# Kernel optimization log

Measured on AMD Instinct MI355X. Metric: run time of the kernel, lower is better.

## Reference

```python
import jax, jax.numpy as jnp
import numpy as np

B, S, D = 4, 4096, 1024
E, K, H = 8, 2, 2048


def setup_inputs() -> dict:
    key = jax.random.key(0)
    ks = jax.random.split(key, 6)
    scale_g = 1.0 / np.sqrt(D)
    scale_1 = 1.0 / np.sqrt(D)
    scale_2 = 1.0 / np.sqrt(H)
    return {
        "x": jax.random.normal(ks[0], (B, S, D), dtype=jnp.float32),
        "Wg": jax.random.uniform(ks[1], (D, E), jnp.float32, -scale_g, scale_g),
        "W1": jax.random.uniform(ks[2], (E, D, H), jnp.float32, -scale_1, scale_1),
        "b1": jax.random.uniform(ks[3], (E, H), jnp.float32, -scale_1, scale_1),
        "W2": jax.random.uniform(ks[4], (E, H, D), jnp.float32, -scale_2, scale_2),
        "b2": jax.random.uniform(ks[5], (E, D), jnp.float32, -scale_2, scale_2),
    }


def reference(x, Wg, W1, b1, W2, b2):
    # Router: softmax gate, top-k selection, renormalized combine weights
    logits = jnp.einsum("bsd,de->bse", x, Wg)          # [B,S,E]
    probs = jax.nn.softmax(logits, axis=-1)
    topv, topi = jax.lax.top_k(probs, K)                # [B,S,K]
    cw = topv / (jnp.sum(topv, axis=-1, keepdims=True) + 1e-9)
    # Per-token weight for each expert: sum over k of one_hot(idx_k)*cw_k -> [B,S,E]
    we = jnp.sum(jax.nn.one_hot(topi, E, dtype=x.dtype) * cw[..., None], axis=-2)
    # Weighted combine of per-expert FFN outputs (loop over small fixed E)
    y = jnp.zeros_like(x)
    for e in range(E):
        h = jax.nn.relu(jnp.einsum("bsd,dh->bsh", x, W1[e]) + b1[e])
        out_e = jnp.einsum("bsh,hd->bsd", h, W2[e]) + b2[e]
        y = y + we[..., e:e + 1] * out_e
    return y
```

## Files before the change

kernel.cpp:

```cpp
#include <hip/hip_runtime.h>
#include <hip/hip_bf16.h>

#define TOK 16384
#define DIM 1024
#define HID 2048
#define NEXP 8

typedef __attribute__((ext_vector_type(4))) float f32x4;
typedef __attribute__((ext_vector_type(8))) short s16x8;

__device__ __forceinline__ unsigned short f2bf(float f) {
  union { float f; unsigned u; } v; v.f = f;
  unsigned r = v.u + 0x7fffu + ((v.u >> 16) & 1u);
  return (unsigned short)(r >> 16);
}
__device__ __forceinline__ int tile_byte(int r, int kk2) {
  return (r * 128 + kk2) ^ ((r & 7) << 4);
}
__device__ __forceinline__ void gld_lds16(const void* g, void* l) {
  __builtin_amdgcn_global_load_lds(
      (const __attribute__((address_space(1))) unsigned int*)g,
      (__attribute__((address_space(3))) unsigned int*)l, 16, 0, 0);
}
__device__ __forceinline__ int xcd_swz(int p, int nwg) {
  int q = nwg >> 3, r = nwg & 7;
  int xcd = p & 7, idx = p >> 3;
  return (xcd < r ? xcd * (q + 1) : r * (q + 1) + (xcd - r) * q) + idx;
}

__global__ void wg_tr(const float* __restrict__ Wg, float* __restrict__ WgT) {
  int i = blockIdx.x * 256 + threadIdx.x;
  int e = i >> 10, dd = i & 1023;
  WgT[i] = Wg[dd * NEXP + e];
}

__global__ void prep_tiles(const float* __restrict__ src, unsigned short* __restrict__ dst,
                           int rows, int cols) {
  int ct = blockIdx.x, kb = blockIdx.y, e = blockIdx.z;
  int nct = gridDim.x, nkb = gridDim.y;
  __shared__ __align__(16) unsigned short tile[8192];
  const float* s = src + ((size_t)e * rows + kb * 64) * cols + ct * 128;
  int tid = threadIdx.x;
  #pragma unroll
  for (int it = 0; it < 8; it++) {
    int idx = it * 256 + tid;
    int kk = idx >> 5;
    int r4 = (idx & 31) * 4;
    float4 v = *(const float4*)(s + (size_t)kk * cols + r4);
    char* tb = (char*)tile;
    *(unsigned short*)(tb + tile_byte(r4 + 0, kk * 2)) = f2bf(v.x);
    *(unsigned short*)(tb + tile_byte(r4 + 1, kk * 2)) = f2bf(v.y);
    *(unsigned short*)(tb + tile_byte(r4 + 2, kk * 2)) = f2bf(v.z);
    *(unsigned short*)(tb + tile_byte(r4 + 3, kk * 2)) = f2bf(v.w);
  }
  __syncthreads();
  unsigned short* d = dst + (((size_t)e * nct + ct) * nkb + kb) * 8192;
  #pragma unroll
  for (int it = 0; it < 4; it++) {
    int o = it * 256 + tid;
    *(s16x8*)(d + o * 8) = *(const s16x8*)((const char*)tile + o * 16);
  }
}

__global__ __launch_bounds__(256)
void router_logits_cvt(const float* __restrict__ x, const float* __restrict__ WgT,
                       unsigned short* __restrict__ xbf,
                       int* __restrict__ sel, float2* __restrict__ wp) {
  int wave = threadIdx.x >> 6, lane = threadIdx.x & 63;
  int t = blockIdx.x * 4 + wave;
  const f32x4* xr = (const f32x4*)(x + (size_t)t * DIM);
  unsigned short* xb = xbf + (size_t)t * DIM;
  float acc[NEXP];
  #pragma unroll
  for (int e = 0; e < NEXP; e++) acc[e] = 0.f;
  #pragma unroll
  for (int q = 0; q < 4; q++) {
    f32x4 xv = xr[q * 64 + lane];
    ushort4 bv;
    bv.x = f2bf(xv[0]); bv.y = f2bf(xv[1]); bv.z = f2bf(xv[2]); bv.w = f2bf(xv[3]);
    *(ushort4*)(xb + (q * 64 + lane) * 4) = bv;
    #pragma unroll
    for (int e = 0; e < NEXP; e++) {
      f32x4 wv = *(const f32x4*)(WgT + (size_t)e * DIM + (q * 64 + lane) * 4);
      acc[e] = fmaf(xv[3], wv[3], fmaf(xv[2], wv[2], fmaf(xv[1], wv[1], fmaf(xv[0], wv[0], acc[e]))));
    }
  }
  #pragma unroll
  for (int e = 0; e < NEXP; e++) {
    float v = acc[e];
    #pragma unroll
    for (int off = 32; off >= 1; off >>= 1) v += __shfl_xor(v, off);
    acc[e] = v;
  }
  if (lane == 0) {
    float m = acc[0];
    #pragma unroll
    for (int e = 1; e < NEXP; e++) m = fmaxf(m, acc[e]);
    float p[NEXP], s = 0.f;
    #pragma unroll
    for (int e = 0; e < NEXP; e++) { p[e] = expf(acc[e] - m); s += p[e]; }
    float inv = 1.f / s;
    int i0 = 0; float v0 = p[0];
    #pragma unroll
    for (int e = 1; e < NEXP; e++) if (p[e] > v0) { v0 = p[e]; i0 = e; }
    int i1 = -1; float v1 = -1.f;
    #pragma unroll
    for (int e = 0; e < NEXP; e++) if (e != i0 && p[e] > v1) { v1 = p[e]; i1 = e; }
    v0 *= inv; v1 *= inv;
    float den = v0 + v1 + 1e-9f;
    sel[t] = i0 | (i1 << 4);
    wp[t] = make_float2(v0 / den, v1 / den);
  }
}

__global__ __launch_bounds__(256)
void router_scatter(const int* __restrict__ sel, const float2* __restrict__ wp,
                    int* __restrict__ counts, int* __restrict__ tok_list,
                    float* __restrict__ w_list) {
  __shared__ int lh0[4][16], lh1[4][16];
  __shared__ int bbase[16];
  int tid = threadIdx.x, wave = tid >> 6, lane = tid & 63;
  int t = blockIdx.x * 256 + tid;
  int s = sel[t];
  int b0 = s & 15;
  int b1 = 8 + ((s >> 4) & 15);
  float2 w = wp[t];
  unsigned long long lt = (lane == 63) ? ~0ull >> 1 : (((unsigned long long)1 << lane) - 1);
  int r0 = 0, r1 = 0;
  #pragma unroll
  for (int b = 0; b < 8; b++) {
    unsigned long long m0 = __ballot(b0 == b);
    if (b0 == b) r0 = __popcll(m0 & lt);
    if (lane == 0) { lh0[wave][b] = __popcll(m0); lh1[wave][b] = 0; }
  }
  #pragma unroll
  for (int b = 8; b < 16; b++) {
    unsigned long long m1 = __ballot(b1 == b);
    if (b1 == b) r1 = __popcll(m1 & lt);
    if (lane == 0) { lh1[wave][b] = __popcll(m1); lh0[wave][b] = 0; }
  }
  __syncthreads();
  if (tid < 16) {
    int h = 0;
    #pragma unroll
    for (int v = 0; v < 4; v++) h += lh0[v][tid] + lh1[v][tid];
    bbase[tid] = atomicAdd(&counts[tid], h);
  }
  __syncthreads();
  int p0 = bbase[b0] + r0;
  int p1 = bbase[b1] + r1;
  #pragma unroll
  for (int v = 0; v < 4; v++) {
    if (v < wave) { p0 += lh0[v][b0]; p1 += lh1[v][b1]; }
  }
  int e0 = b0, e1 = b1 - 8;
  tok_list[e0 * TOK + p0] = t;
  w_list[e0 * TOK + p0] = w.x;
  int q1 = TOK - 1 - p1;
  tok_list[e1 * TOK + q1] = t;
  w_list[e1 * TOK + q1] = w.y;
}

__global__ void calc_off(const int* __restrict__ counts, int* __restrict__ off) {
  if (threadIdx.x == 0 && blockIdx.x == 0) {
    int a = 0;
    for (int e = 0; e < NEXP; e++)
      for (int s = 0; s < 2; s++) {
        off[e * 2 + s] = a;
        a += (counts[s * 8 + e] + 127) & ~127;
      }
  }
}

__global__ __launch_bounds__(256, 4)
void moe_gemm1(const unsigned short* __restrict__ xbf, const unsigned short* __restrict__ w1s,
               const float* __restrict__ b1, const int* __restrict__ counts,
               const int* __restrict__ off, const int* __restrict__ tok_list,
               unsigned short* __restrict__ h_s, int ct_off, int nkbc, int nct) {
  int logical = xcd_swz(blockIdx.x, gridDim.x);
  int ct_l = logical % nct;
  int g = logical / nct;
  int e = -1, seg = 0, rt = 0, segcnt = 0, base = 0;
  #pragma unroll
  for (int zz = 0; zz < 16; zz++) {
    int ee = zz >> 1, ss = zz & 1;
    int c = counts[ss * 8 + ee];
    int nt = (c + 127) >> 7;
    if (e < 0 && g < base + nt) { e = ee; seg = ss; rt = g - base; segcnt = c; }
    base += nt;
  }
  if (e < 0) return;

  __shared__ __align__(16) unsigned short As[8192];
  __shared__ __align__(16) unsigned short Bs[8192];
  __shared__ int tokS[128];

  int tid = threadIdx.x, wave = tid >> 6, lane = tid & 63;
  int llo = lane & 15, lhi = lane >> 4;
  int wr = wave >> 1, wc = wave & 1;
  int ct_g = ct_off + ct_l;

  if (tid < 128) {
    int q = rt * 128 + tid;
    int qq = q < segcnt ? q : segcnt - 1;
    int slot = seg ? (TOK - 1 - qq) : qq;
    tokS[tid] = tok_list[e * TOK + slot];
  }
  __syncthreads();

  const char* srcA[4];
  #pragma unroll
  for (int i = 0; i < 4; i++) {
    int r = i * 32 + (tid >> 3);
    srcA[i] = (const char*)xbf + (size_t)tokS[r] * (DIM * 2) + (((tid & 7) ^ (r & 7)) * 16);
  }
  const char* gB = (const char*)(w1s + (((size_t)e * 16 + ct_g) * 16) * 8192);

  f32x4 acc[4][4];
  #pragma unroll
  for (int i = 0; i < 4; i++)
    #pragma unroll
    for (int j = 0; j < 4; j++) acc[i][j] = (f32x4){0.f, 0.f, 0.f, 0.f};

  for (int kb = 0; kb < 16; kb++) {
    #pragma unroll
    for (int i = 0; i < 4; i++)
      gld_lds16(srcA[i] + kb * 128, (char*)As + i * 4096 + wave * 1024);
    const char* gs = gB + (size_t)kb * 16384 + wave * 1024 + lane * 16;
    #pragma unroll
    for (int i = 0; i < 4; i++)
      gld_lds16(gs + i * 4096, (char*)Bs + i * 4096 + wave * 1024);
    __syncthreads();
    #pragma unroll
    for (int ks = 0; ks < 2; ks++) {
      s16x8 a[4], b[4];
      #pragma unroll
      for (int f = 0; f < 4; f++) {
        a[f] = *(const s16x8*)((const char*)As + tile_byte(wr * 64 + f * 16 + llo, ks * 64 + lhi * 16));
        b[f] = *(const s16x8*)((const char*)Bs + tile_byte(wc * 64 + f * 16 + llo, ks * 64 + lhi * 16));
      }
      #pragma unroll
      for (int fr = 0; fr < 4; fr++)
        #pragma unroll
        for (int fc = 0; fc < 4; fc++)
          acc[fr][fc] = __builtin_amdgcn_mfma_f32_16x16x32_bf16(a[fr], b[fc], acc[fr][fc], 0, 0, 0);
    }
    __syncthreads();
  }

  size_t grt = (size_t)(off[e * 2 + seg] >> 7) + rt;
  unsigned short* hb = h_s + grt * ((size_t)nkbc * 8192);
  const float* b1e = b1 + e * HID + ct_g * 128;
  #pragma unroll
  for (int fc = 0; fc < 4; fc++) {
    int col = wc * 64 + fc * 16 + llo;
    float bv = b1e[col];
    char* tb = (char*)(hb + ((size_t)(ct_l * 2 + (col >> 6))) * 8192);
    int kk2 = (col & 63) * 2;
    #pragma unroll
    for (int fr = 0; fr < 4; fr++) {
      int r0 = wr * 64 + fr * 16 + lhi * 4;
      #pragma unroll
      for (int j = 0; j < 4; j++) {
        float v = fmaxf(acc[fr][fc][j] + bv, 0.f);
        *(unsigned short*)(tb + tile_byte(r0 + j, kk2)) = f2bf(v);
      }
    }
  }
}

template<int NKBC>
__global__ __launch_bounds__(256, 4)
void moe_gemm2(const unsigned short* __restrict__ h_s, const unsigned short* __restrict__ w2s,
               const float* __restrict__ b2, const int* __restrict__ counts,
               const int* __restrict__ off, const int* __restrict__ tok_list,
               const float* __restrict__ w_list, float* __restrict__ y,
               int seg, int kb_off, int add_b2, int accum) {
  int logical = xcd_swz(blockIdx.x, gridDim.x);
  int ct = logical & 7;
  int g = logical >> 3;
  int e = -1, rt = 0, segcnt = 0, base = 0;
  #pragma unroll
  for (int ee = 0; ee < 8; ee++) {
    int c = counts[seg * 8 + ee];
    int nt = (c + 127) >> 7;
    if (e < 0 && g < base + nt) { e = ee; rt = g - base; segcnt = c; }
    base += nt;
  }
  if (e < 0) return;

  __shared__ __align__(16) unsigned short As[8192];
  __shared__ __align__(16) unsigned short Bs[8192];

  int tid = threadIdx.x, wave = tid >> 6, lane = tid & 63;
  int llo = lane & 15, lhi = lane >> 4;
  int wr = wave >> 1, wc = wave & 1;

  size_t grt = (size_t)(off[e * 2 + seg] >> 7) + rt;
  const char* gA = (const char*)(h_s + grt * ((size_t)NKBC * 8192));
  const char* gB = (const char*)(w2s + (((size_t)e * 8 + ct) * 32 + kb_off) * 8192);

  f32x4 acc[4][4];
  #pragma unroll
  for (int i = 0; i < 4; i++)
    #pragma unroll
    for (int j = 0; j < 4; j++) acc[i][j] = (f32x4){0.f, 0.f, 0.f, 0.f};

  for (int kb = 0; kb < NKBC; kb++) {
    const char* ga = gA + (size_t)kb * 16384 + wave * 1024 + lane * 16;
    const char* gb = gB + (size_t)kb * 16384 + wave * 1024 + lane * 16;
    #pragma unroll
    for (int i = 0; i < 4; i++) {
      gld_lds16(ga + i * 4096, (char*)As + i * 4096 + wave * 1024);
      gld_lds16(gb + i * 4096, (char*)Bs + i * 4096 + wave * 1024);
    }
    __syncthreads();
    #pragma unroll
    for (int ks = 0; ks < 2; ks++) {
      s16x8 a[4], b[4];
      #pragma unroll
      for (int f = 0; f < 4; f++) {
        a[f] = *(const s16x8*)((const char*)As + tile_byte(wr * 64 + f * 16 + llo, ks * 64 + lhi * 16));
        b[f] = *(const s16x8*)((const char*)Bs + tile_byte(wc * 64 + f * 16 + llo, ks * 64 + lhi * 16));
      }
      #pragma unroll
      for (int fr = 0; fr < 4; fr++)
        #pragma unroll
        for (int fc = 0; fc < 4; fc++)
          acc[fr][fc] = __builtin_amdgcn_mfma_f32_16x16x32_bf16(a[fr], b[fc], acc[fr][fc], 0, 0, 0);
    }
    __syncthreads();
  }

  const float* b2e = b2 + e * DIM + ct * 128;
  #pragma unroll
  for (int fr = 0; fr < 4; fr++) {
    #pragma unroll
    for (int j = 0; j < 4; j++) {
      int q = rt * 128 + wr * 64 + fr * 16 + lhi * 4 + j;
      if (q < segcnt) {
        int slot = seg ? (TOK - 1 - q) : q;
        int t = tok_list[e * TOK + slot];
        float w = w_list[e * TOK + slot];
        float bs = add_b2 ? w : 0.f;
        #pragma unroll
        for (int fc = 0; fc < 4; fc++) {
          int col = wc * 64 + fc * 16 + llo;
          float val = w * acc[fr][fc][j] + bs * b2e[col];
          size_t idx = (size_t)t * DIM + ct * 128 + col;
          if (accum) y[idx] += val;
          else       y[idx] = val;
        }
      }
    }
  }
}

__global__ void transpose_cvt(const float* __restrict__ src, unsigned short* __restrict__ dst,
                              int R, int C) {
  __shared__ float tile[32][33];
  int e = blockIdx.z;
  const float* s = src + (size_t)e * R * C;
  unsigned short* d = dst + (size_t)e * R * C;
  int c0 = blockIdx.x * 32, r0 = blockIdx.y * 32;
  int tx = threadIdx.x, ty = threadIdx.y;
  #pragma unroll
  for (int i = 0; i < 32; i += 8)
    tile[ty + i][tx] = s[(size_t)(r0 + ty + i) * C + c0 + tx];
  __syncthreads();
  #pragma unroll
  for (int i = 0; i < 32; i += 8)
    d[(size_t)(c0 + ty + i) * R + r0 + tx] = f2bf(tile[tx][ty + i]);
}

__global__ void router_kernel(const float* __restrict__ x, const float* __restrict__ Wg,
                              int* __restrict__ counts, int* __restrict__ tok_list,
                              float* __restrict__ w_list) {
  int wave = threadIdx.x >> 6, lane = threadIdx.x & 63;
  int t = blockIdx.x * 4 + wave;
  const float* xr = x + (size_t)t * DIM;
  float acc[NEXP];
  #pragma unroll
  for (int e = 0; e < NEXP; e++) acc[e] = 0.f;
  for (int i = 0; i < DIM / 64; i++) {
    int dd = i * 64 + lane;
    float xv = xr[dd];
    const float* wr = Wg + (size_t)dd * NEXP;
    #pragma unroll
    for (int e = 0; e < NEXP; e++) acc[e] = fmaf(xv, wr[e], acc[e]);
  }
  #pragma unroll
  for (int e = 0; e < NEXP; e++) {
    float v = acc[e];
    #pragma unroll
    for (int off = 32; off >= 1; off >>= 1) v += __shfl_xor(v, off);
    acc[e] = v;
  }
  if (lane == 0) {
    float m = acc[0];
    #pragma unroll
    for (int e = 1; e < NEXP; e++) m = fmaxf(m, acc[e]);
    float p[NEXP], s = 0.f;
    #pragma unroll
    for (int e = 0; e < NEXP; e++) { p[e] = expf(acc[e] - m); s += p[e]; }
    float inv = 1.f / s;
    int i0 = 0; float v0 = p[0];
    #pragma unroll
    for (int e = 1; e < NEXP; e++) if (p[e] > v0) { v0 = p[e]; i0 = e; }
    int i1 = -1; float v1 = -1.f;
    #pragma unroll
    for (int e = 0; e < NEXP; e++) if (e != i0 && p[e] > v1) { v1 = p[e]; i1 = e; }
    v0 *= inv; v1 *= inv;
    float den = v0 + v1 + 1e-9f;
    float w0 = v0 / den, w1 = v1 / den;
    int q0 = atomicAdd(&counts[i0], 1);
    tok_list[i0 * TOK + q0] = t;           w_list[i0 * TOK + q0] = w0;
    int q1 = atomicAdd(&counts[8 + i1], 1);
    int p1 = TOK - 1 - q1;
    tok_list[i1 * TOK + p1] = t;           w_list[i1 * TOK + p1] = w1;
  }
}

__global__ __launch_bounds__(512, 4)
void moe_ffn_kernel(const float* __restrict__ x,
                    const unsigned short* __restrict__ w1t,
                    const unsigned short* __restrict__ w2t,
                    const float* __restrict__ b1, const float* __restrict__ b2,
                    const int* __restrict__ counts, const int* __restrict__ tok_list,
                    const float* __restrict__ w_list, float* __restrict__ y) {
  int zz = blockIdx.y, e = zz & 7, seg = zz >> 3;
  int segcnt = counts[seg * 8 + e];
  int row0 = blockIdx.x * 32;
  if (row0 >= segcnt) return;
  __shared__ unsigned short Xs[32 * DIM];
  __shared__ unsigned short hsl[32 * 64];
  __shared__ int tokS[32];
  __shared__ float wS[32];
  int tid = threadIdx.x, wave = tid >> 6, lane = tid & 63;
  if (tid < 32) {
    int q = row0 + tid;
    if (q < segcnt) {
      int slot = seg ? (TOK - 1 - q) : q;
      tokS[tid] = tok_list[e * TOK + slot]; wS[tid] = w_list[e * TOK + slot];
    } else { tokS[tid] = -1; wS[tid] = 0.f; }
  }
  __syncthreads();
  #pragma unroll
  for (int it = 0; it < 8; it++) {
    int chunk = it * 512 + tid;
    int r = chunk >> 7, c = (chunk & 127) * 8;
    int tok = tokS[r];
    float4 f0 = make_float4(0.f, 0.f, 0.f, 0.f), f1 = f0;
    if (tok >= 0) {
      const float4* xp = (const float4*)(x + (size_t)tok * DIM + c);
      f0 = xp[0]; f1 = xp[1];
    }
    s16x8 bv;
    bv[0] = (short)f2bf(f0.x); bv[1] = (short)f2bf(f0.y);
    bv[2] = (short)f2bf(f0.z); bv[3] = (short)f2bf(f0.w);
    bv[4] = (short)f2bf(f1.x); bv[5] = (short)f2bf(f1.y);
    bv[6] = (short)f2bf(f1.z); bv[7] = (short)f2bf(f1.w);
    int byte = (r * DIM + c) * 2; byte ^= (r & 7) << 4;
    *(s16x8*)((char*)Xs + byte) = bv;
  }
  __syncthreads();
  int rw = wave >> 2, cw = wave & 3;
  int lhi = lane >> 4, llo = lane & 15;
  f32x4 acc[16];
  #pragma unroll
  for (int i = 0; i < 16; i++) acc[i] = (f32x4){0.f, 0.f, 0.f, 0.f};
  int arow = rw * 16 + llo;
  int abase = arow * (DIM * 2) + lhi * 16;
  int aswz = (arow & 7) << 4;
  int h_abase = arow * (64 * 2) + lhi * 16;
  const size_t eHD = (size_t)e * HID * DIM;
  const unsigned short* w2e = w2t + (size_t)e * DIM * HID;
  for (int hc = 0; hc < HID; hc += 64) {
    f32x4 c1 = (f32x4){0.f, 0.f, 0.f, 0.f};
    const unsigned short* w1p = w1t + eHD + (size_t)(hc + cw * 16 + llo) * DIM + lhi * 8;
    #pragma unroll 4
    for (int k = 0; k < DIM; k += 32) {
      s16x8 a = *(const s16x8*)((const char*)Xs + ((abase + k * 2) ^ aswz));
      s16x8 b = *(const s16x8*)(w1p + k);
      c1 = __builtin_amdgcn_mfma_f32_16x16x32_bf16(a, b, c1, 0, 0, 0);
    }
    float b1v = b1[e * HID + hc + cw * 16 + llo];
    __syncthreads();
    #pragma unroll
    for (int j = 0; j < 4; j++) {
      int r = rw * 16 + lhi * 4 + j;
      float v = fmaxf(c1[j] + b1v, 0.f);
      int byte = (r * 64 + cw * 16 + llo) * 2; byte ^= (r & 7) << 4;
      *(unsigned short*)((char*)hsl + byte) = f2bf(v);
    }
    __syncthreads();
    s16x8 a0 = *(const s16x8*)((const char*)hsl + ((h_abase + 0)  ^ aswz));
    s16x8 a1 = *(const s16x8*)((const char*)hsl + ((h_abase + 64) ^ aswz));
    const unsigned short* w2p0 = w2e + hc + lhi * 8;
    #pragma unroll 4
    for (int ctile = 0; ctile < 16; ctile++) {
      int dcol = cw * 256 + ctile * 16 + llo;
      const unsigned short* bp = w2p0 + (size_t)dcol * HID;
      s16x8 b0 = *(const s16x8*)(bp);
      s16x8 b1f = *(const s16x8*)(bp + 32);
      acc[ctile] = __builtin_amdgcn_mfma_f32_16x16x32_bf16(a0, b0, acc[ctile], 0, 0, 0);
      acc[ctile] = __builtin_amdgcn_mfma_f32_16x16x32_bf16(a1, b1f, acc[ctile], 0, 0, 0);
    }
  }
  const float* b2e = b2 + e * DIM;
  #pragma unroll
  for (int ctile = 0; ctile < 16; ctile++) {
    int dcol = cw * 256 + ctile * 16 + llo;
    float b2v = b2e[dcol];
    #pragma unroll
    for (int j = 0; j < 4; j++) {
      int r = rw * 16 + lhi * 4 + j;
      int tok = tokS[r];
      if (tok >= 0) atomicAdd(&y[(size_t)tok * DIM + dcol], wS[r] * (acc[ctile][j] + b2v));
    }
  }
}

extern "C" void kernel_launch(void* const* d_in, const int* in_sizes, int n_in,
                              void* d_out, int out_size, void* d_ws, size_t ws_size,
                              hipStream_t stream) {
  const float* x  = (const float*)d_in[0];
  const float* Wg = (const float*)d_in[1];
  const float* W1 = (const float*)d_in[2];
  const float* b1 = (const float*)d_in[3];
  const float* W2 = (const float*)d_in[4];
  const float* b2 = (const float*)d_in[5];
  float* y = (float*)d_out;
  char* ws = (char*)d_ws;

  const size_t O_COUNTS = 0;
  const size_t O_OFF    = 1024;
  const size_t O_TOK    = 2048;
  const size_t O_W      = O_TOK + (size_t)NEXP * TOK * 4;
  const size_t O_WGT    = O_W + (size_t)NEXP * TOK * 4;
  const size_t O_SEL    = O_WGT + (size_t)NEXP * DIM * 4;
  const size_t O_WP     = O_SEL + (size_t)TOK * 4;
  const size_t O_W1S    = O_WP + (size_t)TOK * 8;
  const size_t O_W2S    = O_W1S + (size_t)NEXP * 16 * 16 * 8192 * 2;
  const size_t O_XBF    = O_W2S + (size_t)NEXP * 8 * 32 * 8192 * 2;
  const size_t O_HS     = O_XBF + (size_t)TOK * DIM * 2;

  int Hc = 0;
  if (ws_size > O_HS) {
    size_t avail = ws_size - O_HS;
    for (int hc = HID; hc >= 128; hc >>= 1)
      if ((size_t)34816 * hc * 2 <= avail) { Hc = hc; break; }
  }

  if (Hc) {
    int*   counts   = (int*)(ws + O_COUNTS);
    int*   offp     = (int*)(ws + O_OFF);
    int*   tok_list = (int*)(ws + O_TOK);
    float* w_list   = (float*)(ws + O_W);
    float* WgT      = (float*)(ws + O_WGT);
    int*   sel      = (int*)(ws + O_SEL);
    float2* wp      = (float2*)(ws + O_WP);
    unsigned short* w1s = (unsigned short*)(ws + O_W1S);
    unsigned short* w2s = (unsigned short*)(ws + O_W2S);
    unsigned short* xbf = (unsigned short*)(ws + O_XBF);
    unsigned short* hs  = (unsigned short*)(ws + O_HS);

    hipMemsetAsync(counts, 0, 2048, stream);
    wg_tr<<<32, 256, 0, stream>>>(Wg, WgT);
    prep_tiles<<<dim3(HID / 128, DIM / 64, NEXP), 256, 0, stream>>>(W1, w1s, DIM, HID);
    prep_tiles<<<dim3(DIM / 128, HID / 64, NEXP), 256, 0, stream>>>(W2, w2s, HID, DIM);
    router_logits_cvt<<<TOK / 4, 256, 0, stream>>>(x, WgT, xbf, sel, wp);
    router_scatter<<<TOK / 256, 256, 0, stream>>>(sel, wp, counts, tok_list, w_list);
    calc_off<<<1, 64, 0, stream>>>(counts, offp);

    int nch = HID / Hc, nkbc = Hc / 64, nct = Hc / 128;
    for (int ch = 0; ch < nch; ch++) {
      moe_gemm1<<<272 * nct, 256, 0, stream>>>(
          xbf, w1s, b1, counts, offp, tok_list, hs, ch * nct, nkbc, nct);
      for (int seg = 0; seg < 2; seg++) {
        int add_b2 = (ch == 0) ? 1 : 0;
        int accum  = (ch == 0 && seg == 0) ? 0 : 1;
        int kb_off = ch * nkbc;
        #define LG2(NK) moe_gemm2<NK><<<136 * 8, 256, 0, stream>>>( \
            hs, w2s, b2, counts, offp, tok_list, w_list, y, seg, kb_off, add_b2, accum)
        switch (nkbc) {
          case 32: LG2(32); break;
          case 16: LG2(16); break;
          case 8:  LG2(8);  break;
          case 4:  LG2(4);  break;
          default: LG2(2);  break;
        }
        #undef LG2
      }
    }
  } else {
    int*   counts   = (int*)ws;
    int*   tok_list = (int*)(ws + 2048);
    float* w_list   = (float*)(ws + 2048 + (size_t)NEXP * TOK * 4);
    unsigned short* w1t = (unsigned short*)(ws + 2048 + (size_t)NEXP * TOK * 8);
    unsigned short* w2t = w1t + (size_t)NEXP * HID * DIM;

    hipMemsetAsync(d_out, 0, (size_t)out_size * sizeof(float), stream);
    hipMemsetAsync(counts, 0, 2048, stream);
    transpose_cvt<<<dim3(HID / 32, DIM / 32, NEXP), dim3(32, 8), 0, stream>>>(W1, w1t, DIM, HID);
    transpose_cvt<<<dim3(DIM / 32, HID / 32, NEXP), dim3(32, 8), 0, stream>>>(W2, w2t, HID, DIM);
    router_kernel<<<TOK / 4, 256, 0, stream>>>(x, Wg, counts, tok_list, w_list);
    moe_ffn_kernel<<<dim3(TOK / 32, 16), 512, 0, stream>>>(
        x, w1t, w2t, b1, b2, counts, tok_list, w_list, y);
  }
}
```

Baseline: 513.4 us.

## Double-buffer LDS tiles in both MoE GEMMs to overlap loads with MFMA

```diff
diff --git a/kernel.cpp b/kernel.cpp
--- a/kernel.cpp
+++ b/kernel.cpp
@@ -172,7 +172,7 @@
   }
 }
 
-__global__ __launch_bounds__(256, 4)
+__global__ __launch_bounds__(256, 2)
 void moe_gemm1(const unsigned short* __restrict__ xbf, const unsigned short* __restrict__ w1s,
                const float* __restrict__ b1, const int* __restrict__ counts,
                const int* __restrict__ off, const int* __restrict__ tok_list,
@@ -191,8 +191,8 @@
   }
   if (e < 0) return;
 
-  __shared__ __align__(16) unsigned short As[8192];
-  __shared__ __align__(16) unsigned short Bs[8192];
+  __shared__ __align__(16) unsigned short As[2][8192];
+  __shared__ __align__(16) unsigned short Bs[2][8192];
   __shared__ int tokS[128];
 
   int tid = threadIdx.x, wave = tid >> 6, lane = tid & 63;
@@ -222,22 +222,30 @@
     #pragma unroll
     for (int j = 0; j < 4; j++) acc[i][j] = (f32x4){0.f, 0.f, 0.f, 0.f};
 
+  auto stage = [&](int buf, int kb) {
+    #pragma unroll
+    for (int i = 0; i < 4; i++)
+      gld_lds16(srcA[i] + kb * 128, (char*)As[buf] + i * 4096 + wave * 1024);
+    const char* gs = gB + (size_t)kb * 16384 + wave * 1024 + lane * 16;
+    #pragma unroll
+    for (int i = 0; i < 4; i++)
+      gld_lds16(gs + i * 4096, (char*)Bs[buf] + i * 4096 + wave * 1024);
+  };
+
+  stage(0, 0);
+  __syncthreads();
   for (int kb = 0; kb < 16; kb++) {
-    #pragma unroll
-    for (int i = 0; i < 4; i++)
-      gld_lds16(srcA[i] + kb * 128, (char*)As + i * 4096 + wave * 1024);
-    const char* gs = gB + (size_t)kb * 16384 + wave * 1024 + lane * 16;
-    #pragma unroll
-    for (int i = 0; i < 4; i++)
-      gld_lds16(gs + i * 4096, (char*)Bs + i * 4096 + wave * 1024);
-    __syncthreads();
+    int cur = kb & 1;
+    if (kb < 15) stage(cur ^ 1, kb + 1);
+    const char* Ab = (const char*)As[cur];
+    const char* Bb = (const char*)Bs[cur];
     #pragma unroll
     for (int ks = 0; ks < 2; ks++) {
       s16x8 a[4], b[4];
       #pragma unroll
       for (int f = 0; f < 4; f++) {
-        a[f] = *(const s16x8*)((const char*)As + tile_byte(wr * 64 + f * 16 + llo, ks * 64 + lhi * 16));
-        b[f] = *(const s16x8*)((const char*)Bs + tile_byte(wc * 64 + f * 16 + llo, ks * 64 + lhi * 16));
+        a[f] = *(const s16x8*)(Ab + tile_byte(wr * 64 + f * 16 + llo, ks * 64 + lhi * 16));
+        b[f] = *(const s16x8*)(Bb + tile_byte(wc * 64 + f * 16 + llo, ks * 64 + lhi * 16));
       }
       #pragma unroll
       for (int fr = 0; fr < 4; fr++)
@@ -270,7 +278,7 @@
 }
 
 template<int NKBC>
-__global__ __launch_bounds__(256, 4)
+__global__ __launch_bounds__(256, 2)
 void moe_gemm2(const unsigned short* __restrict__ h_s, const unsigned short* __restrict__ w2s,
                const float* __restrict__ b2, const int* __restrict__ counts,
                const int* __restrict__ off, const int* __restrict__ tok_list,
@@ -289,8 +297,8 @@
   }
   if (e < 0) return;
 
-  __shared__ __align__(16) unsigned short As[8192];
-  __shared__ __align__(16) unsigned short Bs[8192];
+  __shared__ __align__(16) unsigned short As[2][8192];
+  __shared__ __align__(16) unsigned short Bs[2][8192];
 
   int tid = threadIdx.x, wave = tid >> 6, lane = tid & 63;
   int llo = lane & 15, lhi = lane >> 4;
@@ -306,22 +314,30 @@
     #pragma unroll
     for (int j = 0; j < 4; j++) acc[i][j] = (f32x4){0.f, 0.f, 0.f, 0.f};
 
-  for (int kb = 0; kb < NKBC; kb++) {
+  auto stage = [&](int buf, int kb) {
     const char* ga = gA + (size_t)kb * 16384 + wave * 1024 + lane * 16;
     const char* gb = gB + (size_t)kb * 16384 + wave * 1024 + lane * 16;
     #pragma unroll
     for (int i = 0; i < 4; i++) {
-      gld_lds16(ga + i * 4096, (char*)As + i * 4096 + wave * 1024);
-      gld_lds16(gb + i * 4096, (char*)Bs + i * 4096 + wave * 1024);
-    }
-    __syncthreads();
+      gld_lds16(ga + i * 4096, (char*)As[buf] + i * 4096 + wave * 1024);
+      gld_lds16(gb + i * 4096, (char*)Bs[buf] + i * 4096 + wave * 1024);
+    }
+  };
+
+  stage(0, 0);
+  __syncthreads();
+  for (int kb = 0; kb < NKBC; kb++) {
+    int cur = kb & 1;
+    if (kb + 1 < NKBC) stage(cur ^ 1, kb + 1);
+    const char* Ab = (const char*)As[cur];
+    const char* Bb = (const char*)Bs[cur];
     #pragma unroll
     for (int ks = 0; ks < 2; ks++) {
       s16x8 a[4], b[4];
       #pragma unroll
       for (int f = 0; f < 4; f++) {
-        a[f] = *(const s16x8*)((const char*)As + tile_byte(wr * 64 + f * 16 + llo, ks * 64 + lhi * 16));
-        b[f] = *(const s16x8*)((const char*)Bs + tile_byte(wc * 64 + f * 16 + llo, ks * 64 + lhi * 16));
+        a[f] = *(const s16x8*)(Ab + tile_byte(wr * 64 + f * 16 + llo, ks * 64 + lhi * 16));
+        b[f] = *(const s16x8*)(Bb + tile_byte(wc * 64 + f * 16 + llo, ks * 64 + lhi * 16));
       }
       #pragma unroll
       for (int fr = 0; fr < 4; fr++)
```

New measurement: 629.4 us. +22.6%, slower.
